# Optimization experiments

Hardware: AMD Instinct MI355X
Metric: run time of the kernel (lower is better)

Reference implementation:

```python
import jax, jax.numpy as jnp
import numpy as np

D_MODEL, N_HEADS, D_FFN = 256, 8, 1024
HEAD_DIM = D_MODEL // N_HEADS
BZ, H, W = 2, 56, 56
EPS = 1e-5


def _layer_norm(x, g, b):
    m = jnp.mean(x, axis=-1, keepdims=True)
    v = jnp.mean((x - m) ** 2, axis=-1, keepdims=True)
    return (x - m) / jnp.sqrt(v + EPS) * g + b


def _forward(src, posemb_row, posemb_col,
             w_q_row, b_q_row, w_q_col, b_q_col,
             w_k_row, b_k_row, w_k_col, b_k_col,
             w_v, b_v, w_out, b_out,
             norm1_g, norm1_b, lin1_w, lin1_b, lin2_w, lin2_b,
             norm2_g, norm2_b, padding_mask):
    bz, c, h, w = src.shape
    nq = h * w
    x = src.transpose(0, 2, 3, 1)                      # (b,h,w,c)
    x_pr = x + posemb_row[:, None, :, :]               # row posemb broadcast over h
    x_pc = x + posemb_col[:, :, None, :]               # col posemb broadcast over w
    scaling = HEAD_DIM ** -0.5

    q_row = (x_pr.reshape(bz, nq, c) @ w_q_row.T + b_q_row) * scaling
    q_col = (x_pc.reshape(bz, nq, c) @ w_q_col.T + b_q_col) * scaling
    k_row = (x_pr @ w_k_row.T + b_k_row).mean(axis=1)  # (b,w,c): pool over rows
    k_col = (x_pc @ w_k_col.T + b_k_col).mean(axis=2)  # (b,h,c): pool over cols
    v = x @ w_v.T + b_v                                # (b,h,w,c)

    q_row = q_row.reshape(bz, nq, N_HEADS, HEAD_DIM)
    q_col = q_col.reshape(bz, nq, N_HEADS, HEAD_DIM)
    k_row = k_row.reshape(bz, w, N_HEADS, HEAD_DIM)
    k_col = k_col.reshape(bz, h, N_HEADS, HEAD_DIM)
    v = v.reshape(bz, h, w, N_HEADS, HEAD_DIM)

    aw_row = jnp.einsum('bqnd,bwnd->bnqw', q_row, k_row)
    aw_col = jnp.einsum('bqnd,bhnd->bnqh', q_col, k_col)
    neg = jnp.finfo(aw_row.dtype).min
    aw_row = jnp.where(padding_mask[:, 0, :][:, None, None, :], neg, aw_row)
    aw_col = jnp.where(padding_mask[:, :, 0][:, None, None, :], neg, aw_col)
    aw_row = jax.nn.softmax(aw_row, axis=-1)
    aw_col = jax.nn.softmax(aw_col, axis=-1)

    # out[q] = sum_h A_col[q,h] * (sum_w A_row[q,w] * V[h,w])  (RCDA recombination)
    tmp = jnp.einsum('bnqw,bhwnd->bnqhd', aw_row, v)   # dominant intermediate
    attn = jnp.einsum('bnqh,bnqhd->bqnd', aw_col, tmp).reshape(bz, nq, c)
    attn = attn @ w_out.T + b_out                      # (b,hw,c)

    x = _layer_norm(x + attn.reshape(bz, h, w, c), norm1_g, norm1_b)
    y = jax.nn.relu(x @ lin1_w.T + lin1_b) @ lin2_w.T + lin2_b
    x = _layer_norm(x + y, norm2_g, norm2_b)
    return x.transpose(0, 3, 1, 2)                     # (b,c,h,w)


def setup_inputs() -> dict:
    key = jax.random.key(0)
    ks = jax.random.split(key, 12)

    def wmat(k, shape, scale=0.02):
        return jax.random.normal(k, shape, jnp.float32) * scale

    return {
        'src': jax.random.normal(ks[0], (BZ, D_MODEL, H, W), jnp.float32),
        'padding_mask': jnp.zeros((BZ, H, W), jnp.bool_),
        'posemb_row': jax.random.normal(ks[1], (BZ, W, D_MODEL), jnp.float32),
        'posemb_col': jax.random.normal(ks[2], (BZ, H, D_MODEL), jnp.float32),
        'w_q_row': wmat(ks[3], (D_MODEL, D_MODEL)),
        'b_q_row': jnp.zeros((D_MODEL,), jnp.float32),
        'w_q_col': wmat(ks[4], (D_MODEL, D_MODEL)),
        'b_q_col': jnp.zeros((D_MODEL,), jnp.float32),
        'w_k_row': wmat(ks[5], (D_MODEL, D_MODEL)),
        'b_k_row': jnp.zeros((D_MODEL,), jnp.float32),
        'w_k_col': wmat(ks[6], (D_MODEL, D_MODEL)),
        'b_k_col': jnp.zeros((D_MODEL,), jnp.float32),
        'w_v': wmat(ks[7], (D_MODEL, D_MODEL)),
        'b_v': jnp.zeros((D_MODEL,), jnp.float32),
        'w_out': wmat(ks[8], (D_MODEL, D_MODEL)),
        'b_out': jnp.zeros((D_MODEL,), jnp.float32),
        'norm1_g': jnp.ones((D_MODEL,), jnp.float32),
        'norm1_b': jnp.zeros((D_MODEL,), jnp.float32),
        'lin1_w': wmat(ks[9], (D_FFN, D_MODEL)),
        'lin1_b': jnp.zeros((D_FFN,), jnp.float32),
        'lin2_w': wmat(ks[10], (D_MODEL, D_FFN)),
        'lin2_b': jnp.zeros((D_MODEL,), jnp.float32),
        'norm2_g': jnp.ones((D_MODEL,), jnp.float32),
        'norm2_b': jnp.zeros((D_MODEL,), jnp.float32),
    }


def reference(src, padding_mask, posemb_row, posemb_col,
              w_q_row, b_q_row, w_q_col, b_q_col,
              w_k_row, b_k_row, w_k_col, b_k_col,
              w_v, b_v, w_out, b_out,
              norm1_g, norm1_b, lin1_w, lin1_b, lin2_w, lin2_b,
              norm2_g, norm2_b):
    return _forward(src, posemb_row, posemb_col,
                    w_q_row, b_q_row, w_q_col, b_q_col,
                    w_k_row, b_k_row, w_k_col, b_k_col,
                    w_v, b_v, w_out, b_out,
                    norm1_g, norm1_b, lin1_w, lin1_b, lin2_w, lin2_b,
                    norm2_g, norm2_b, padding_mask)
```

## Files before the change

### kernel.cpp

```cpp
#include <hip/hip_runtime.h>
#include <math.h>

#define EPSV 1e-5f
#define SCALV 0.17677669529663687f

typedef __attribute__((ext_vector_type(8))) short s16x8;
typedef __attribute__((ext_vector_type(8))) __bf16 bf8_t;
typedef __attribute__((ext_vector_type(4))) float f32x4;

__device__ inline unsigned short f2bfu(float f) {
  union { float f; unsigned u; } v; v.f = f;
  return (unsigned short)((v.u + 0x7FFFu + ((v.u >> 16) & 1u)) >> 16);
}

__device__ inline f32x4 mfma16(s16x8 a, s16x8 b, f32x4 c) {
  return __builtin_amdgcn_mfma_f32_16x16x32_bf16(
      __builtin_bit_cast(bf8_t, a), __builtin_bit_cast(bf8_t, b), c, 0, 0, 0);
}

__device__ inline void gll16(const void* g, const void* l) {
  __builtin_amdgcn_global_load_lds(
      (const __attribute__((address_space(1))) unsigned*)g,
      (__attribute__((address_space(3))) unsigned*)l, 16, 0, 0);
}

__global__ __launch_bounds__(256) void k_prep0(
    const float* __restrict__ src,
    const float* __restrict__ wqr, const float* __restrict__ wqc, const float* __restrict__ wv,
    const float* __restrict__ wo, const float* __restrict__ l1w, const float* __restrict__ l2w,
    float* __restrict__ X, short* __restrict__ Xb,
    short* __restrict__ Wcat, short* __restrict__ wob,
    short* __restrict__ l1b, short* __restrict__ l2b) {
  __shared__ float tile[32][33];
  int bid = blockIdx.x;
  int tid = threadIdx.x;
  if (bid < 1568) {
    int b = bid / 784;
    int rem = bid - b * 784;
    int cb = rem / 98, hwb = rem % 98;
    int hw0 = hwb * 32, c0 = cb * 32;
    int tx = tid & 31, ty = tid >> 5;
    for (int i = ty; i < 32; i += 8)
      tile[i][tx] = src[((size_t)(b * 256 + c0 + i)) * 3136 + hw0 + tx];
    __syncthreads();
    for (int i = ty; i < 32; i += 8) {
      float v = tile[tx][i];
      size_t idx = ((size_t)(b * 3136 + hw0 + i)) * 256 + c0 + tx;
      X[idx] = v;
      Xb[idx] = (short)f2bfu(v);
    }
  } else {
    int pb = bid - 1568;
    int seg = pb >> 8;
    int e = (((pb & 255) * 256) + tid) * 4;
    int cnt = (seg == 0) ? 196608 : (seg == 1) ? 65536 : 262144;
    if (e >= cnt) return;
    const float* sp;
    short* dp;
    if (seg == 0) {
      dp = Wcat + e;
      sp = (e < 65536) ? wqr + e : (e < 131072) ? wqc + (e - 65536) : wv + (e - 131072);
    } else if (seg == 1) { dp = wob + e; sp = wo + e; }
    else if (seg == 2)   { dp = l1b + e; sp = l1w + e; }
    else                 { dp = l2b + e; sp = l2w + e; }
    float4 v = *(const float4*)sp;
    uint2 p;
    p.x = (unsigned)f2bfu(v.x) | ((unsigned)f2bfu(v.y) << 16);
    p.y = (unsigned)f2bfu(v.z) | ((unsigned)f2bfu(v.w) << 16);
    *(uint2*)dp = p;
  }
}

__global__ __launch_bounds__(256) void k_smallproj2(
    const float* __restrict__ per, const float* __restrict__ pec,
    const float* __restrict__ X,
    const float* __restrict__ wqr, const float* __restrict__ wqc,
    const float* __restrict__ wkr, const float* __restrict__ wkc,
    const float* __restrict__ bkr, const float* __restrict__ bkc,
    float* __restrict__ PRW, float* __restrict__ PCW,
    float* __restrict__ KR, float* __restrict__ KC) {
  __shared__ __align__(16) float inb[256];
  int s = blockIdx.x / 112;
  int r = blockIdx.x % 112;
  int j = threadIdx.x;
  const float* W;
  const float* bias = nullptr;
  float* out;
  float v;
  if (s == 0) {
    v = per[(size_t)r * 256 + j]; W = wqr; out = PRW;
  } else if (s == 1) {
    v = pec[(size_t)r * 256 + j]; W = wqc; out = PCW;
  } else if (s == 2) {
    int b = r / 56, w = r % 56;
    float sum = 0.f;
    for (int h = 0; h < 56; ++h)
      sum += X[((size_t)(b * 3136 + h * 56 + w)) * 256 + j];
    v = per[(size_t)r * 256 + j] + sum * (1.f / 56.f);
    W = wkr; bias = bkr; out = KR;
  } else {
    int b = r / 56, h = r % 56;
    float sum = 0.f;
    for (int w = 0; w < 56; ++w)
      sum += X[((size_t)(b * 3136 + h * 56 + w)) * 256 + j];
    v = pec[(size_t)r * 256 + j] + sum * (1.f / 56.f);
    W = wkc; bias = bkc; out = KC;
  }
  inb[j] = v;
  __syncthreads();
  const float* wrow = W + (size_t)j * 256;
  float acc = 0.f;
  #pragma unroll
  for (int c4 = 0; c4 < 64; ++c4) {
    float4 iv = *(const float4*)(&inb[c4 * 4]);
    float4 wv = *(const float4*)(wrow + c4 * 4);
    acc += iv.x * wv.x + iv.y * wv.y + iv.z * wv.z + iv.w * wv.w;
  }
  if (bias) acc += bias[j];
  out[(size_t)r * 256 + j] = acc;
}

#define GEMM64_CORE(Aptr, Wptr, Kdim)                                           \
  __shared__ __align__(16) short Ls[2][2][4096];                                \
  int tid = threadIdx.x;                                                        \
  int wid = tid >> 6, lane = tid & 63;                                          \
  int ln15 = lane & 15, slot = lane >> 4;                                       \
  int m0 = blockIdx.x * 64, n0 = blockIdx.y * 64;                               \
  int l8 = lane >> 3, c8 = lane & 7;                                            \
  int csw = ((c8 ^ l8) << 4);                                                   \
  int K2 = (Kdim) * 2;                                                          \
  const char* Ag = (const char*)(Aptr) + (size_t)(m0 + wid * 16 + l8) * K2 + csw; \
  const char* Wg = (const char*)(Wptr) + (size_t)(n0 + wid * 16 + l8) * K2 + csw; \
  int u0 = __builtin_amdgcn_readfirstlane(wid * 2048);                          \
  int wm0 = (wid >> 1) << 5, wn0 = (wid & 1) << 5;                              \
  int xr = ln15 & 7;                                                            \
  f32x4 acc[2][2] = {};                                                         \
  int nt = (Kdim) >> 6;                                                         \
  {                                                                             \
    char* bA = (char*)&Ls[0][0][0];                                             \
    char* bB = (char*)&Ls[0][1][0];                                             \
    gll16(Ag, bA + u0);                                                         \
    gll16(Ag + (size_t)8 * K2, bA + u0 + 1024);                                 \
    gll16(Wg, bB + u0);                                                         \
    gll16(Wg + (size_t)8 * K2, bB + u0 + 1024);                                 \
  }                                                                             \
  __syncthreads();                                                              \
  for (int t = 0; t < nt; ++t) {                                                \
    int bf = t & 1;                                                             \
    if (t + 1 < nt) {                                                           \
      size_t ko = (size_t)(t + 1) * 128;                                        \
      char* bA = (char*)&Ls[bf ^ 1][0][0];                                      \
      char* bB = (char*)&Ls[bf ^ 1][1][0];                                      \
      gll16(Ag + ko, bA + u0);                                                  \
      gll16(Ag + ko + (size_t)8 * K2, bA + u0 + 1024);                          \
      gll16(Wg + ko, bB + u0);                                                  \
      gll16(Wg + ko + (size_t)8 * K2, bB + u0 + 1024);                          \
    }                                                                           \
    const char* LA = (const char*)&Ls[bf][0][0];                                \
    const char* LB = (const char*)&Ls[bf][1][0];                                \
    _Pragma("unroll")                                                           \
    for (int kc = 0; kc < 2; ++kc) {                                            \
      s16x8 af[2], bv2[2];                                                      \
      _Pragma("unroll")                                                         \
      for (int mf = 0; mf < 2; ++mf)                                            \
        af[mf] = *(const s16x8*)(LA + (wm0 + mf * 16 + ln15) * 128              \
                                  + (((kc * 4 + slot) ^ xr) << 4));             \
      _Pragma("unroll")                                                         \
      for (int nf = 0; nf < 2; ++nf)                                            \
        bv2[nf] = *(const s16x8*)(LB + (wn0 + nf * 16 + ln15) * 128             \
                                   + (((kc * 4 + slot) ^ xr) << 4));            \
      _Pragma("unroll")                                                         \
      for (int mf = 0; mf < 2; ++mf)                                            \
        _Pragma("unroll")                                                       \
        for (int nf = 0; nf < 2; ++nf)                                          \
          acc[mf][nf] = mfma16(af[mf], bv2[nf], acc[mf][nf]);                   \
    }                                                                           \
    __syncthreads();                                                            \
  }

template<int EPI>
__global__ __launch_bounds__(256) void k_gemm64p(
    const short* __restrict__ A, const short* __restrict__ W,
    const float* __restrict__ bias, float* __restrict__ outF,
    short* __restrict__ outB, int K, int N) {
  GEMM64_CORE(A, W, K)
  #pragma unroll
  for (int mf = 0; mf < 2; ++mf)
    #pragma unroll
    for (int nf = 0; nf < 2; ++nf) {
      int gc = n0 + wn0 + (nf << 4) + ln15;
      float bs = bias[gc];
      #pragma unroll
      for (int r = 0; r < 4; ++r) {
        int gr = m0 + wm0 + (mf << 4) + (slot << 2) + r;
        float v = acc[mf][nf][r] + bs;
        if (EPI == 0) outF[(size_t)gr * N + gc] = v;
        else          outB[(size_t)gr * N + gc] = (short)f2bfu(fmaxf(v, 0.f));
      }
    }
}

__global__ __launch_bounds__(256) void k_proj64p(
    const short* __restrict__ A, const short* __restrict__ W,
    const float* __restrict__ bqr, const float* __restrict__ bqc, const float* __restrict__ bv,
    const float* __restrict__ PRW, const float* __restrict__ PCW,
    float* __restrict__ QR, float* __restrict__ QC, short* __restrict__ Vt) {
  GEMM64_CORE(A, W, 256)
  int s = n0 >> 8;
  #pragma unroll
  for (int mf = 0; mf < 2; ++mf)
    #pragma unroll
    for (int nf = 0; nf < 2; ++nf) {
      f32x4 c = acc[mf][nf];
      int gc = n0 + wn0 + (nf << 4) + ln15;
      int jl = gc & 255;
      #pragma unroll
      for (int r = 0; r < 4; ++r) {
        int gr = m0 + wm0 + (mf << 4) + (slot << 2) + r;
        int bb = gr >= 3136;
        int q = gr - bb * 3136;
        if (s == 0) {
          int w = q % 56;
          QR[(size_t)gr * 256 + jl] =
              (c[r] + PRW[((size_t)(bb * 56 + w)) * 256 + jl] + bqr[jl]) * SCALV;
        } else if (s == 1) {
          int h = q / 56;
          QC[(size_t)gr * 256 + jl] =
              (c[r] + PCW[((size_t)(bb * 56 + h)) * 256 + jl] + bqc[jl]) * SCALV;
        } else {
          int nn = jl >> 5, d = jl & 31;
          int h = q / 56, w = q - h * 56;
          Vt[((size_t)((bb * 8 + nn) * 32 + d)) * 3584 + h * 64 + w] =
              (short)f2bfu(c[r] + bv[jl]);
        }
      }
    }
}

__global__ __launch_bounds__(256, 2) void k_fattn2(
    const float* __restrict__ QR, const float* __restrict__ QC,
    const float* __restrict__ KR, const float* __restrict__ KC,
    const unsigned char* __restrict__ pm,
    const short* __restrict__ Vt, short* __restrict__ ATTb) {
  __shared__ __align__(16) short KsRb[64 * 32];
  __shared__ __align__(16) short KsCb[64 * 32];
  __shared__ __align__(16) short Ar[128 * 72];
  __shared__ __align__(16) short Acs[128 * 56];
  __shared__ __align__(16) short Vs[4 * 2176];
  int tid = threadIdx.x;
  int wid = tid >> 6, lane = tid & 63;
  int ln15 = lane & 15, slot = lane >> 4;
  int q0 = blockIdx.x * 128;
  int n = blockIdx.y, b = blockIdx.z;
  int bn = b * 8 + n;
  for (int l = tid; l < 64 * 32; l += 256) {
    int row = l >> 5, d = l & 31;
    float vr = 0.f, vc = 0.f;
    if (row < 56) {
      vr = KR[((size_t)(b * 56 + row) << 8) + (n << 5) + d];
      vc = KC[((size_t)(b * 56 + row) << 8) + (n << 5) + d];
    }
    KsRb[l] = (short)f2bfu(vr);
    KsCb[l] = (short)f2bfu(vc);
  }
  for (int l = tid; l < 128 * 16; l += 256) {
    int q = l >> 4, c = 56 + (l & 15);
    Ar[q * 72 + c] = 0;
  }
  __syncthreads();
  bool mr[4], mc[4];
  #pragma unroll
  for (int nf = 0; nf < 4; ++nf) {
    int c = nf * 16 + ln15;
    if (c >= 56) { mr[nf] = true; mc[nf] = true; }
    else {
      mr[nf] = pm[(size_t)b * 3136 + c] != 0;
      mc[nf] = pm[(size_t)b * 3136 + c * 56] != 0;
    }
  }
  #pragma unroll
  for (int side = 0; side < 2; ++side) {
    const float* Qg = side ? QC : QR;
    const short* Kb = side ? KsCb : KsRb;
    const bool* mk = side ? mc : mr;
    s16x8 qa[2];
    #pragma unroll
    for (int mf = 0; mf < 2; ++mf) {
      int q = q0 + wid * 32 + mf * 16 + ln15; if (q > 3135) q = 3135;
      const float* qp = Qg + ((size_t)(b * 3136 + q) << 8) + (n << 5) + slot * 8;
      float4 t0 = *(const float4*)qp;
      float4 t1 = *(const float4*)(qp + 4);
      s16x8 f;
      f[0] = (short)f2bfu(t0.x); f[1] = (short)f2bfu(t0.y);
      f[2] = (short)f2bfu(t0.z); f[3] = (short)f2bfu(t0.w);
      f[4] = (short)f2bfu(t1.x); f[5] = (short)f2bfu(t1.y);
      f[6] = (short)f2bfu(t1.z); f[7] = (short)f2bfu(t1.w);
      qa[mf] = f;
    }
    s16x8 kb[4];
    #pragma unroll
    for (int nf = 0; nf < 4; ++nf)
      kb[nf] = *(const s16x8*)(Kb + (nf * 16 + ln15) * 32 + slot * 8);
    f32x4 sacc[2][4];
    #pragma unroll
    for (int mf = 0; mf < 2; ++mf)
      #pragma unroll
      for (int nf = 0; nf < 4; ++nf) {
        f32x4 z = {0.f, 0.f, 0.f, 0.f};
        sacc[mf][nf] = mfma16(qa[mf], kb[nf], z);
      }
    #pragma unroll
    for (int mf = 0; mf < 2; ++mf)
      #pragma unroll
      for (int r = 0; r < 4; ++r) {
        float v[4];
        #pragma unroll
        for (int nf = 0; nf < 4; ++nf)
          v[nf] = mk[nf] ? -3.402823466e38f : sacc[mf][nf][r];
        float m = fmaxf(fmaxf(v[0], v[1]), fmaxf(v[2], v[3]));
        #pragma unroll
        for (int o = 1; o < 16; o <<= 1) m = fmaxf(m, __shfl_xor(m, o));
        float e[4], ss = 0.f;
        #pragma unroll
        for (int nf = 0; nf < 4; ++nf) {
          e[nf] = mk[nf] ? 0.f : __expf(v[nf] - m);
          ss += e[nf];
        }
        #pragma unroll
        for (int o = 1; o < 16; o <<= 1) ss += __shfl_xor(ss, o);
        float inv = 1.f / ss;
        int ql = wid * 32 + mf * 16 + slot * 4 + r;
        if (side == 0) {
          #pragma unroll
          for (int nf = 0; nf < 4; ++nf) {
            int c = nf * 16 + ln15;
            if (c < 56) Ar[ql * 72 + c] = (short)f2bfu(e[nf] * inv);
          }
        } else {
          #pragma unroll
          for (int nf = 0; nf < 4; ++nf) {
            int c = nf * 16 + ln15;
            if (c < 56) Acs[ql * 56 + c] = (short)f2bfu(e[nf] * inv);
          }
        }
      }
  }
  const short* Vg = Vt + (size_t)bn * 32 * 3584;
  int sd = (tid >> 3) & 31, swp = tid & 7;
  const short* vsrc = Vg + (size_t)sd * 3584 + swp * 8;
  short* vdst = Vs + sd * 68 + swp * 8;
  s16x8 pre[4];
  #pragma unroll
  for (int i = 0; i < 4; ++i)
    pre[i] = *(const s16x8*)(vsrc + (size_t)i * 64);
  #pragma unroll
  for (int i = 0; i < 4; ++i)
    *(s16x8*)(vdst + i * 2176) = pre[i];
  __syncthreads();
  s16x8 bfr[2][2];
  #pragma unroll
  for (int qf = 0; qf < 2; ++qf)
    #pragma unroll
    for (int kc = 0; kc < 2; ++kc)
      bfr[qf][kc] = *(const s16x8*)(Ar + (wid * 32 + qf * 16 + ln15) * 72
                                       + kc * 32 + slot * 8);
  f32x4 oacc[2][2] = {};
  for (int hc = 0; hc < 14; ++hc) {
    if (hc < 13) {
      #pragma unroll
      for (int i = 0; i < 4; ++i)
        pre[i] = *(const s16x8*)(vsrc + (size_t)((hc + 1) * 4 + i) * 64);
    }
    #pragma unroll
    for (int hh = 0; hh < 4; ++hh) {
      int h = hc * 4 + hh;
      s16x8 af[2][2];
      #pragma unroll
      for (int df = 0; df < 2; ++df)
        #pragma unroll
        for (int kc = 0; kc < 2; ++kc)
          af[df][kc] = *(const s16x8*)(Vs + hh * 2176 + (df * 16 + ln15) * 68
                                          + kc * 32 + slot * 8);
      #pragma unroll
      for (int qf = 0; qf < 2; ++qf) {
        float acv = __uint_as_float(
            ((unsigned)(unsigned short)Acs[(wid * 32 + qf * 16 + ln15) * 56 + h]) << 16);
        #pragma unroll
        for (int df = 0; df < 2; ++df) {
          f32x4 tmp = {0.f, 0.f, 0.f, 0.f};
          tmp = mfma16(af[df][0], bfr[qf][0], tmp);
          tmp = mfma16(af[df][1], bfr[qf][1], tmp);
          oacc[df][qf][0] += acv * tmp[0];
          oacc[df][qf][1] += acv * tmp[1];
          oacc[df][qf][2] += acv * tmp[2];
          oacc[df][qf][3] += acv * tmp[3];
        }
      }
    }
    if (hc < 13) {
      __syncthreads();
      #pragma unroll
      for (int i = 0; i < 4; ++i)
        *(s16x8*)(vdst + i * 2176) = pre[i];
      __syncthreads();
    }
  }
  __syncthreads();
  #pragma unroll
  for (int df = 0; df < 2; ++df)
    #pragma unroll
    for (int qf = 0; qf < 2; ++qf) {
      int qi = wid * 32 + qf * 16 + ln15;
      short4 pk;
      pk.x = (short)f2bfu(oacc[df][qf][0]);
      pk.y = (short)f2bfu(oacc[df][qf][1]);
      pk.z = (short)f2bfu(oacc[df][qf][2]);
      pk.w = (short)f2bfu(oacc[df][qf][3]);
      *(short4*)(Ar + qi * 36 + df * 16 + slot * 4) = pk;
    }
  __syncthreads();
  int q = tid >> 1, half = tid & 1;
  int qg = q0 + q;
  if (qg < 3136) {
    s16x8 v = *(const s16x8*)(Ar + q * 36 + half * 16);
    *(s16x8*)(ATTb + ((size_t)(b * 3136 + qg)) * 256 + n * 32 + half * 16) = v;
  }
}

__global__ __launch_bounds__(256) void k_ln1(
    const float* __restrict__ Y, const float* __restrict__ X,
    const float* __restrict__ g, const float* __restrict__ bb,
    float* __restrict__ XN1f, short* __restrict__ XN1b) {
  int tid = threadIdx.x;
  int row = blockIdx.x * 4 + (tid >> 6);
  int ln = tid & 63;
  size_t base = (size_t)row * 256 + ln * 4;
  float4 y = *(const float4*)(Y + base);
  float4 x = *(const float4*)(X + base);
  float v0 = y.x + x.x, v1 = y.y + x.y, v2 = y.z + x.z, v3 = y.w + x.w;
  float s = v0 + v1 + v2 + v3;
  float s2 = v0 * v0 + v1 * v1 + v2 * v2 + v3 * v3;
  for (int o = 32; o; o >>= 1) { s += __shfl_xor(s, o); s2 += __shfl_xor(s2, o); }
  float m = s * (1.f / 256.f);
  float inv = rsqrtf(fmaxf(s2 * (1.f / 256.f) - m * m, 0.f) + EPSV);
  float4 gg = *(const float4*)(g + ln * 4);
  float4 bv = *(const float4*)(bb + ln * 4);
  float4 o4;
  o4.x = (v0 - m) * inv * gg.x + bv.x;
  o4.y = (v1 - m) * inv * gg.y + bv.y;
  o4.z = (v2 - m) * inv * gg.z + bv.z;
  o4.w = (v3 - m) * inv * gg.w + bv.w;
  *(float4*)(XN1f + base) = o4;
  uint2 pk;
  pk.x = (unsigned)f2bfu(o4.x) | ((unsigned)f2bfu(o4.y) << 16);
  pk.y = (unsigned)f2bfu(o4.z) | ((unsigned)f2bfu(o4.w) << 16);
  *(uint2*)(XN1b + base) = pk;
}

__global__ __launch_bounds__(256) void k_ln2t(
    const float* __restrict__ Y2, const float* __restrict__ XN1,
    const float* __restrict__ g, const float* __restrict__ bb,
    float* __restrict__ out) {
  __shared__ float VL[16][257];
  int tid = threadIdx.x;
  int r0 = blockIdx.x * 16;
  for (int l = tid; l < 16 * 256; l += 256) {
    int r = l >> 8, c = l & 255;
    VL[r][c] = Y2[(size_t)(r0 + r) * 256 + c] + XN1[(size_t)(r0 + r) * 256 + c];
  }
  __syncthreads();
  int wv = tid >> 6, ln = tid & 63;
  for (int rr = wv; rr < 16; rr += 4) {
    float s = 0.f, s2 = 0.f;
    float vv[4];
    #pragma unroll
    for (int i = 0; i < 4; ++i) {
      float v = VL[rr][ln * 4 + i];
      vv[i] = v; s += v; s2 += v * v;
    }
    for (int o = 32; o; o >>= 1) { s += __shfl_xor(s, o); s2 += __shfl_xor(s2, o); }
    float m = s * (1.f / 256.f);
    float inv = rsqrtf(fmaxf(s2 * (1.f / 256.f) - m * m, 0.f) + EPSV);
    #pragma unroll
    for (int i = 0; i < 4; ++i) {
      int c = ln * 4 + i;
      VL[rr][c] = (vv[i] - m) * inv * g[c] + bb[c];
    }
  }
  __syncthreads();
  int b = r0 / 3136;
  int hw0 = r0 % 3136;
  int r = tid & 15, cg = tid >> 4;
  for (int it = 0; it < 16; ++it) {
    int c = it * 16 + cg;
    out[(size_t)(b * 256 + c) * 3136 + hw0 + r] = VL[r][c];
  }
}

extern "C" void kernel_launch(void* const* d_in, const int* in_sizes, int n_in,
                              void* d_out, int out_size, void* d_ws, size_t ws_size,
                              hipStream_t stream) {
  const float* src = (const float*)d_in[0];
  const unsigned char* pmask = (const unsigned char*)d_in[1];
  const float* per = (const float*)d_in[2];
  const float* pec = (const float*)d_in[3];
  const float* wqr = (const float*)d_in[4];
  const float* bqr = (const float*)d_in[5];
  const float* wqc = (const float*)d_in[6];
  const float* bqc = (const float*)d_in[7];
  const float* wkr = (const float*)d_in[8];
  const float* bkr = (const float*)d_in[9];
  const float* wkc = (const float*)d_in[10];
  const float* bkc = (const float*)d_in[11];
  const float* wv  = (const float*)d_in[12];
  const float* bv  = (const float*)d_in[13];
  const float* wo  = (const float*)d_in[14];
  const float* bo  = (const float*)d_in[15];
  const float* n1g = (const float*)d_in[16];
  const float* n1b = (const float*)d_in[17];
  const float* l1w = (const float*)d_in[18];
  const float* l1b = (const float*)d_in[19];
  const float* l2w = (const float*)d_in[20];
  const float* l2b = (const float*)d_in[21];
  const float* n2g = (const float*)d_in[22];
  const float* n2b = (const float*)d_in[23];

  float* ws = (float*)d_ws;
  float* X    = ws + 0;
  short* Xb   = (short*)(ws + 1605632);
  float* QR   = ws + 2408448;
  float* QC   = ws + 4014080;
  short* Vt   = (short*)(ws + 5619712);
  short* ATTb = (short*)(ws + 12156928);
  short* FFb  = (short*)(ws + 12959744);
  float* Y    = ws + 16171008;
  float* XN1f = ws + 17776640;
  short* XN1b = (short*)(ws + 19382272);
  float* PRW  = ws + 20242432;
  float* PCW  = ws + 20271104;
  float* KR   = ws + 20299776;
  float* KC   = ws + 20328448;
  short* Wcat = (short*)(ws + 20357120);
  short* wob  = (short*)(ws + 20455424);
  short* l1wb = (short*)(ws + 20488192);
  short* l2wb = (short*)(ws + 20619264);
  float* out = (float*)d_out;

  k_prep0<<<2592, 256, 0, stream>>>(src, wqr, wqc, wv, wo, l1w, l2w,
                                    X, Xb, Wcat, wob, l1wb, l2wb);
  k_smallproj2<<<448, 256, 0, stream>>>(per, pec, X, wqr, wqc, wkr, wkc,
                                        bkr, bkc, PRW, PCW, KR, KC);
  k_proj64p<<<dim3(98, 12), 256, 0, stream>>>(Xb, Wcat, bqr, bqc, bv,
                                              PRW, PCW, QR, QC, Vt);
  k_fattn2<<<dim3(25, 8, 2), 256, 0, stream>>>(QR, QC, KR, KC, pmask, Vt, ATTb);
  k_gemm64p<0><<<dim3(98, 4), 256, 0, stream>>>(ATTb, wob, bo, Y, nullptr, 256, 256);
  k_ln1<<<1568, 256, 0, stream>>>(Y, X, n1g, n1b, XN1f, XN1b);
  k_gemm64p<1><<<dim3(98, 16), 256, 0, stream>>>(XN1b, l1wb, l1b, nullptr, FFb, 256, 1024);
  k_gemm64p<0><<<dim3(98, 4), 256, 0, stream>>>(FFb, l2wb, l2b, Y, nullptr, 1024, 256);
  k_ln2t<<<392, 256, 0, stream>>>(Y, XN1f, n2g, n2b, out);
}
```

Before: 213.2 us.

## Fuse output and FFN2 GEMMs with LayerNorm, merge prep and small-projection kernels

Adds a k_gemm_ln kernel that computes full 256-column rows per block (32 rows × 256 cols) and applies bias, residual add and LayerNorm in the epilogue. The second instance also does the transposed NCHW output store. This replaces the separate Y round-trip and the k_ln1/k_ln2t kernels. The small pooled-K/posemb projections are folded into the prep kernel and now read src directly, so the fp32 X copy is dropped and the first residual uses bf16 Xb. The risks are lower residual precision and only 196 blocks for the fused GEMMs, which may underfill the GPU.

After: 236.8 us. 1.11x slower.

```diff
diff --git a/kernel.cpp b/kernel.cpp
--- a/kernel.cpp
+++ b/kernel.cpp
@@ -11,6 +11,9 @@
 __device__ inline unsigned short f2bfu(float f) {
   union { float f; unsigned u; } v; v.f = f;
   return (unsigned short)((v.u + 0x7FFFu + ((v.u >> 16) & 1u)) >> 16);
+}
+__device__ inline float bf2f(short s) {
+  return __uint_as_float(((unsigned)(unsigned short)s) << 16);
 }
 
 __device__ inline f32x4 mfma16(s16x8 a, s16x8 b, f32x4 c) {
@@ -24,14 +27,20 @@
       (__attribute__((address_space(3))) unsigned*)l, 16, 0, 0);
 }
 
-__global__ __launch_bounds__(256) void k_prep0(
+__global__ __launch_bounds__(256) void k_prep(
     const float* __restrict__ src,
+    const float* __restrict__ per, const float* __restrict__ pec,
     const float* __restrict__ wqr, const float* __restrict__ wqc, const float* __restrict__ wv,
     const float* __restrict__ wo, const float* __restrict__ l1w, const float* __restrict__ l2w,
-    float* __restrict__ X, short* __restrict__ Xb,
+    const float* __restrict__ wkr, const float* __restrict__ wkc,
+    const float* __restrict__ bkr, const float* __restrict__ bkc,
+    short* __restrict__ Xb,
     short* __restrict__ Wcat, short* __restrict__ wob,
-    short* __restrict__ l1b, short* __restrict__ l2b) {
+    short* __restrict__ l1wb, short* __restrict__ l2wb,
+    float* __restrict__ PRW, float* __restrict__ PCW,
+    float* __restrict__ KR, float* __restrict__ KC) {
   __shared__ float tile[32][33];
+  __shared__ __align__(16) float inb[256];
   int bid = blockIdx.x;
   int tid = threadIdx.x;
   if (bid < 1568) {
@@ -44,12 +53,10 @@
       tile[i][tx] = src[((size_t)(b * 256 + c0 + i)) * 3136 + hw0 + tx];
     __syncthreads();
     for (int i = ty; i < 32; i += 8) {
-      float v = tile[tx][i];
       size_t idx = ((size_t)(b * 3136 + hw0 + i)) * 256 + c0 + tx;
-      X[idx] = v;
-      Xb[idx] = (short)f2bfu(v);
-    }
-  } else {
+      Xb[idx] = (short)f2bfu(tile[tx][i]);
+    }
+  } else if (bid < 2592) {
     int pb = bid - 1568;
     int seg = pb >> 8;
     int e = (((pb & 255) * 256) + tid) * 4;
@@ -61,63 +68,53 @@
       dp = Wcat + e;
       sp = (e < 65536) ? wqr + e : (e < 131072) ? wqc + (e - 65536) : wv + (e - 131072);
     } else if (seg == 1) { dp = wob + e; sp = wo + e; }
-    else if (seg == 2)   { dp = l1b + e; sp = l1w + e; }
-    else                 { dp = l2b + e; sp = l2w + e; }
+    else if (seg == 2)   { dp = l1wb + e; sp = l1w + e; }
+    else                 { dp = l2wb + e; sp = l2w + e; }
     float4 v = *(const float4*)sp;
     uint2 p;
     p.x = (unsigned)f2bfu(v.x) | ((unsigned)f2bfu(v.y) << 16);
     p.y = (unsigned)f2bfu(v.z) | ((unsigned)f2bfu(v.w) << 16);
     *(uint2*)dp = p;
-  }
-}
-
-__global__ __launch_bounds__(256) void k_smallproj2(
-    const float* __restrict__ per, const float* __restrict__ pec,
-    const float* __restrict__ X,
-    const float* __restrict__ wqr, const float* __restrict__ wqc,
-    const float* __restrict__ wkr, const float* __restrict__ wkc,
-    const float* __restrict__ bkr, const float* __restrict__ bkc,
-    float* __restrict__ PRW, float* __restrict__ PCW,
-    float* __restrict__ KR, float* __restrict__ KC) {
-  __shared__ __align__(16) float inb[256];
-  int s = blockIdx.x / 112;
-  int r = blockIdx.x % 112;
-  int j = threadIdx.x;
-  const float* W;
-  const float* bias = nullptr;
-  float* out;
-  float v;
-  if (s == 0) {
-    v = per[(size_t)r * 256 + j]; W = wqr; out = PRW;
-  } else if (s == 1) {
-    v = pec[(size_t)r * 256 + j]; W = wqc; out = PCW;
-  } else if (s == 2) {
-    int b = r / 56, w = r % 56;
-    float sum = 0.f;
-    for (int h = 0; h < 56; ++h)
-      sum += X[((size_t)(b * 3136 + h * 56 + w)) * 256 + j];
-    v = per[(size_t)r * 256 + j] + sum * (1.f / 56.f);
-    W = wkr; bias = bkr; out = KR;
   } else {
-    int b = r / 56, h = r % 56;
-    float sum = 0.f;
-    for (int w = 0; w < 56; ++w)
-      sum += X[((size_t)(b * 3136 + h * 56 + w)) * 256 + j];
-    v = pec[(size_t)r * 256 + j] + sum * (1.f / 56.f);
-    W = wkc; bias = bkc; out = KC;
-  }
-  inb[j] = v;
-  __syncthreads();
-  const float* wrow = W + (size_t)j * 256;
-  float acc = 0.f;
-  #pragma unroll
-  for (int c4 = 0; c4 < 64; ++c4) {
-    float4 iv = *(const float4*)(&inb[c4 * 4]);
-    float4 wv = *(const float4*)(wrow + c4 * 4);
-    acc += iv.x * wv.x + iv.y * wv.y + iv.z * wv.z + iv.w * wv.w;
-  }
-  if (bias) acc += bias[j];
-  out[(size_t)r * 256 + j] = acc;
+    int sb = bid - 2592;
+    int s = sb / 112, r = sb % 112;
+    int j = tid;
+    const float* W;
+    const float* bias = nullptr;
+    float* out;
+    float v;
+    if (s == 0) {
+      v = per[(size_t)r * 256 + j]; W = wqr; out = PRW;
+    } else if (s == 1) {
+      v = pec[(size_t)r * 256 + j]; W = wqc; out = PCW;
+    } else if (s == 2) {
+      int b = r / 56, w = r % 56;
+      const float* p = src + ((size_t)(b * 256 + j)) * 3136 + w;
+      float sum = 0.f;
+      for (int h = 0; h < 56; ++h) sum += p[h * 56];
+      v = per[(size_t)r * 256 + j] + sum * (1.f / 56.f);
+      W = wkr; bias = bkr; out = KR;
+    } else {
+      int b = r / 56, h = r % 56;
+      const float* p = src + ((size_t)(b * 256 + j)) * 3136 + h * 56;
+      float sum = 0.f;
+      for (int w = 0; w < 56; ++w) sum += p[w];
+      v = pec[(size_t)r * 256 + j] + sum * (1.f / 56.f);
+      W = wkc; bias = bkc; out = KC;
+    }
+    inb[j] = v;
+    __syncthreads();
+    const float* wrow = W + (size_t)j * 256;
+    float acc = 0.f;
+    #pragma unroll
+    for (int c4 = 0; c4 < 64; ++c4) {
+      float4 iv = *(const float4*)(&inb[c4 * 4]);
+      float4 wv4 = *(const float4*)(wrow + c4 * 4);
+      acc += iv.x * wv4.x + iv.y * wv4.y + iv.z * wv4.z + iv.w * wv4.w;
+    }
+    if (bias) acc += bias[j];
+    out[(size_t)r * 256 + j] = acc;
+  }
 }
 
 #define GEMM64_CORE(Aptr, Wptr, Kdim)                                           \
@@ -383,8 +380,7 @@
                                           + kc * 32 + slot * 8);
       #pragma unroll
       for (int qf = 0; qf < 2; ++qf) {
-        float acv = __uint_as_float(
-            ((unsigned)(unsigned short)Acs[(wid * 32 + qf * 16 + ln15) * 56 + h]) << 16);
+        float acv = bf2f(Acs[(wid * 32 + qf * 16 + ln15) * 56 + h]);
         #pragma unroll
         for (int df = 0; df < 2; ++df) {
           f32x4 tmp = {0.f, 0.f, 0.f, 0.f};
@@ -427,73 +423,130 @@
   }
 }
 
-__global__ __launch_bounds__(256) void k_ln1(
-    const float* __restrict__ Y, const float* __restrict__ X,
+template<int TRANS>
+__global__ __launch_bounds__(256, 2) void k_gemm_ln(
+    const short* __restrict__ A, const short* __restrict__ W,
+    const float* __restrict__ bias, const void* __restrict__ resid,
     const float* __restrict__ g, const float* __restrict__ bb,
-    float* __restrict__ XN1f, short* __restrict__ XN1b) {
+    float* __restrict__ outF, short* __restrict__ outB,
+    float* __restrict__ outT, int K) {
+  __shared__ __align__(16) char arena[73728];
+  __shared__ float prt[2][32][2];
   int tid = threadIdx.x;
-  int row = blockIdx.x * 4 + (tid >> 6);
-  int ln = tid & 63;
-  size_t base = (size_t)row * 256 + ln * 4;
-  float4 y = *(const float4*)(Y + base);
-  float4 x = *(const float4*)(X + base);
-  float v0 = y.x + x.x, v1 = y.y + x.y, v2 = y.z + x.z, v3 = y.w + x.w;
-  float s = v0 + v1 + v2 + v3;
-  float s2 = v0 * v0 + v1 * v1 + v2 * v2 + v3 * v3;
-  for (int o = 32; o; o >>= 1) { s += __shfl_xor(s, o); s2 += __shfl_xor(s2, o); }
-  float m = s * (1.f / 256.f);
-  float inv = rsqrtf(fmaxf(s2 * (1.f / 256.f) - m * m, 0.f) + EPSV);
-  float4 gg = *(const float4*)(g + ln * 4);
-  float4 bv = *(const float4*)(bb + ln * 4);
-  float4 o4;
-  o4.x = (v0 - m) * inv * gg.x + bv.x;
-  o4.y = (v1 - m) * inv * gg.y + bv.y;
-  o4.z = (v2 - m) * inv * gg.z + bv.z;
-  o4.w = (v3 - m) * inv * gg.w + bv.w;
-  *(float4*)(XN1f + base) = o4;
-  uint2 pk;
-  pk.x = (unsigned)f2bfu(o4.x) | ((unsigned)f2bfu(o4.y) << 16);
-  pk.y = (unsigned)f2bfu(o4.z) | ((unsigned)f2bfu(o4.w) << 16);
-  *(uint2*)(XN1b + base) = pk;
-}
-
-__global__ __launch_bounds__(256) void k_ln2t(
-    const float* __restrict__ Y2, const float* __restrict__ XN1,
-    const float* __restrict__ g, const float* __restrict__ bb,
-    float* __restrict__ out) {
-  __shared__ float VL[16][257];
-  int tid = threadIdx.x;
-  int r0 = blockIdx.x * 16;
-  for (int l = tid; l < 16 * 256; l += 256) {
-    int r = l >> 8, c = l & 255;
-    VL[r][c] = Y2[(size_t)(r0 + r) * 256 + c] + XN1[(size_t)(r0 + r) * 256 + c];
+  int wid = tid >> 6, lane = tid & 63;
+  int ln15 = lane & 15, slot = lane >> 4;
+  int wm = wid >> 1, wn = wid & 1;
+  int m0 = blockIdx.x * 32;
+  int l8 = lane >> 3, c8 = lane & 7;
+  int csw = ((c8 ^ l8) << 4);
+  int K2 = K * 2;
+  const char* Ag = (const char*)A + (size_t)(m0 + wid * 8 + l8) * K2 + csw;
+  const char* Wg = (const char*)W + (size_t)(wid * 8 + l8) * K2 + csw;
+  int uu = __builtin_amdgcn_readfirstlane(wid * 1024);
+  f32x4 acc[8] = {};
+  int nt = K >> 6;
+  {
+    char* bA = arena;
+    char* bB = arena + 8192;
+    gll16(Ag, bA + uu);
+    #pragma unroll
+    for (int i = 0; i < 8; ++i)
+      gll16(Wg + (size_t)(i * 32) * K2, bB + uu + i * 4096);
   }
   __syncthreads();
-  int wv = tid >> 6, ln = tid & 63;
-  for (int rr = wv; rr < 16; rr += 4) {
-    float s = 0.f, s2 = 0.f;
-    float vv[4];
-    #pragma unroll
-    for (int i = 0; i < 4; ++i) {
-      float v = VL[rr][ln * 4 + i];
-      vv[i] = v; s += v; s2 += v * v;
-    }
-    for (int o = 32; o; o >>= 1) { s += __shfl_xor(s, o); s2 += __shfl_xor(s2, o); }
-    float m = s * (1.f / 256.f);
-    float inv = rsqrtf(fmaxf(s2 * (1.f / 256.f) - m * m, 0.f) + EPSV);
-    #pragma unroll
-    for (int i = 0; i < 4; ++i) {
-      int c = ln * 4 + i;
-      VL[rr][c] = (vv[i] - m) * inv * g[c] + bb[c];
+  for (int t = 0; t < nt; ++t) {
+    int bf = t & 1;
+    if (t + 1 < nt) {
+      size_t ko = (size_t)(t + 1) * 128;
+      char* bA = arena + ((bf ^ 1) << 12);
+      char* bB = arena + 8192 + ((bf ^ 1) << 15);
+      gll16(Ag + ko, bA + uu);
+      #pragma unroll
+      for (int i = 0; i < 8; ++i)
+        gll16(Wg + ko + (size_t)(i * 32) * K2, bB + uu + i * 4096);
+    }
+    const char* LA = arena + (bf << 12);
+    const char* LB = arena + 8192 + (bf << 15);
+    #pragma unroll
+    for (int kc = 0; kc < 2; ++kc) {
+      int co = (((kc * 4 + slot) ^ (ln15 & 7)) << 4);
+      s16x8 af = *(const s16x8*)(LA + (wm * 16 + ln15) * 128 + co);
+      #pragma unroll
+      for (int nf = 0; nf < 8; ++nf) {
+        s16x8 bv2 = *(const s16x8*)(LB + (wn * 128 + nf * 16 + ln15) * 128 + co);
+        acc[nf] = mfma16(af, bv2, acc[nf]);
+      }
+    }
+    __syncthreads();
+  }
+  float vv[8][4];
+  float s1[4] = {0.f, 0.f, 0.f, 0.f}, sq[4] = {0.f, 0.f, 0.f, 0.f};
+  #pragma unroll
+  for (int nf = 0; nf < 8; ++nf) {
+    int col = wn * 128 + nf * 16 + ln15;
+    float bs = bias[col];
+    #pragma unroll
+    for (int r = 0; r < 4; ++r) {
+      int row = m0 + wm * 16 + slot * 4 + r;
+      float x = TRANS ? ((const float*)resid)[(size_t)row * 256 + col]
+                      : bf2f(((const short*)resid)[(size_t)row * 256 + col]);
+      float v = acc[nf][r] + bs + x;
+      vv[nf][r] = v;
+      s1[r] += v;
+      sq[r] += v * v;
+    }
+  }
+  #pragma unroll
+  for (int off = 1; off < 16; off <<= 1)
+    #pragma unroll
+    for (int r = 0; r < 4; ++r) {
+      s1[r] += __shfl_xor(s1[r], off);
+      sq[r] += __shfl_xor(sq[r], off);
+    }
+  if (ln15 == 0) {
+    #pragma unroll
+    for (int r = 0; r < 4; ++r) {
+      int lr = wm * 16 + slot * 4 + r;
+      prt[wn][lr][0] = s1[r];
+      prt[wn][lr][1] = sq[r];
     }
   }
   __syncthreads();
-  int b = r0 / 3136;
-  int hw0 = r0 % 3136;
-  int r = tid & 15, cg = tid >> 4;
-  for (int it = 0; it < 16; ++it) {
-    int c = it * 16 + cg;
-    out[(size_t)(b * 256 + c) * 3136 + hw0 + r] = VL[r][c];
+  float* VL = (float*)arena;
+  #pragma unroll
+  for (int r = 0; r < 4; ++r) {
+    int lr = wm * 16 + slot * 4 + r;
+    float S = prt[0][lr][0] + prt[1][lr][0];
+    float Q = prt[0][lr][1] + prt[1][lr][1];
+    float mu = S * (1.f / 256.f);
+    float inv = rsqrtf(fmaxf(Q * (1.f / 256.f) - mu * mu, 0.f) + EPSV);
+    #pragma unroll
+    for (int nf = 0; nf < 8; ++nf) {
+      int col = wn * 128 + nf * 16 + ln15;
+      float o = (vv[nf][r] - mu) * inv * g[col] + bb[col];
+      if (TRANS == 0) {
+        size_t idx = (size_t)(m0 + lr) * 256 + col;
+        outF[idx] = o;
+        outB[idx] = (short)f2bfu(o);
+      } else {
+        VL[lr * 258 + col] = o;
+      }
+    }
+  }
+  if (TRANS == 1) {
+    __syncthreads();
+    int b = m0 / 3136;
+    int q0 = m0 % 3136;
+    float* op = outT + ((size_t)(b * 256 + tid)) * 3136 + q0;
+    #pragma unroll
+    for (int q4 = 0; q4 < 8; ++q4) {
+      float4 v4;
+      v4.x = VL[(q4 * 4 + 0) * 258 + tid];
+      v4.y = VL[(q4 * 4 + 1) * 258 + tid];
+      v4.z = VL[(q4 * 4 + 2) * 258 + tid];
+      v4.w = VL[(q4 * 4 + 3) * 258 + tid];
+      *(float4*)(op + q4 * 4) = v4;
+    }
   }
 }
 
@@ -526,36 +579,33 @@
   const float* n2b = (const float*)d_in[23];
 
   float* ws = (float*)d_ws;
-  float* X    = ws + 0;
-  short* Xb   = (short*)(ws + 1605632);
-  float* QR   = ws + 2408448;
-  float* QC   = ws + 4014080;
-  short* Vt   = (short*)(ws + 5619712);
-  short* ATTb = (short*)(ws + 12156928);
-  short* FFb  = (short*)(ws + 12959744);
-  float* Y    = ws + 16171008;
-  float* XN1f = ws + 17776640;
-  short* XN1b = (short*)(ws + 19382272);
-  float* PRW  = ws + 20242432;
-  float* PCW  = ws + 20271104;
-  float* KR   = ws + 20299776;
-  float* KC   = ws + 20328448;
-  short* Wcat = (short*)(ws + 20357120);
-  short* wob  = (short*)(ws + 20455424);
-  short* l1wb = (short*)(ws + 20488192);
-  short* l2wb = (short*)(ws + 20619264);
+  short* Xb   = (short*)(ws + 0);
+  float* QR   = ws + 802816;
+  float* QC   = ws + 2408448;
+  short* Vt   = (short*)(ws + 4014080);
+  short* ATTb = (short*)(ws + 4931584);
+  short* FFb  = (short*)(ws + 5734400);
+  float* XN1f = ws + 8945664;
+  short* XN1b = (short*)(ws + 10551296);
+  float* PRW  = ws + 11354112;
+  float* PCW  = ws + 11382784;
+  float* KR   = ws + 11411456;
+  float* KC   = ws + 11440128;
+  short* Wcat = (short*)(ws + 11468800);
+  short* wob  = (short*)(ws + 11567104);
+  short* l1wb = (short*)(ws + 11599872);
+  short* l2wb = (short*)(ws + 11730944);
   float* out = (float*)d_out;
 
-  k_prep0<<<2592, 256, 0, stream>>>(src, wqr, wqc, wv, wo, l1w, l2w,
-                                    X, Xb, Wcat, wob, l1wb, l2wb);
-  k_smallproj2<<<448, 256, 0, stream>>>(per, pec, X, wqr, wqc, wkr, wkc,
-                                        bkr, bkc, PRW, PCW, KR, KC);
+  k_prep<<<3040, 256, 0, stream>>>(src, per, pec, wqr, wqc, wv, wo, l1w, l2w,
+                                   wkr, wkc, bkr, bkc, Xb, Wcat, wob, l1wb, l2wb,
+                                   PRW, PCW, KR, KC);
   k_proj64p<<<dim3(98, 12), 256, 0, stream>>>(Xb, Wcat, bqr, bqc, bv,
                                               PRW, PCW, QR, QC, Vt);
   k_fattn2<<<dim3(25, 8, 2), 256, 0, stream>>>(QR, QC, KR, KC, pmask, Vt, ATTb);
-  k_gemm64p<0><<<dim3(98, 4), 256, 0, stream>>>(ATTb, wob, bo, Y, nullptr, 256, 256);
-  k_ln1<<<1568, 256, 0, stream>>>(Y, X, n1g, n1b, XN1f, XN1b);
+  k_gemm_ln<0><<<196, 256, 0, stream>>>(ATTb, wob, bo, Xb, n1g, n1b,
+                                        XN1f, XN1b, nullptr, 256);
   k_gemm64p<1><<<dim3(98, 16), 256, 0, stream>>>(XN1b, l1wb, l1b, nullptr, FFb, 256, 1024);
-  k_gemm64p<0><<<dim3(98, 4), 256, 0, stream>>>(FFb, l2wb, l2b, Y, nullptr, 1024, 256);
-  k_ln2t<<<392, 256, 0, stream>>>(Y, XN1f, n2g, n2b, out);
-}
+  k_gemm_ln<1><<<196, 256, 0, stream>>>(FFb, l2wb, l2b, XN1f, n2g, n2b,
+                                        nullptr, nullptr, out, 1024);
+}
```
